# Performance work log

Measured on AMD Instinct MI355X. Metric: run time of the kernel, lower is better.

Reference implementation:

```python
import jax, jax.numpy as jnp
import numpy as np

HEADS = 8
DIM_HEAD = 32
EPS = 1e-5


def setup_inputs() -> dict:
    key = jax.random.key(0)
    ks = jax.random.split(key, 6)
    B, C, N = 2, 256, 2048
    inner = HEADS * DIM_HEAD  # 256
    return {
        "x": jax.random.normal(ks[0], (B, C, N), dtype=jnp.float32),
        "gamma": jnp.ones((C,), dtype=jnp.float32),
        "beta": jnp.zeros((C,), dtype=jnp.float32),
        "wk": jax.random.normal(ks[1], (inner, C // HEADS), dtype=jnp.float32) * 0.05,
        "wq": jax.random.normal(ks[2], (inner, C // HEADS), dtype=jnp.float32) * 0.05,
        "wv": jax.random.normal(ks[3], (inner, C // HEADS), dtype=jnp.float32) * 0.05,
        "wo": jax.random.normal(ks[4], (C, inner), dtype=jnp.float32) * 0.05,
        "bo": jnp.zeros((C,), dtype=jnp.float32),
    }


def reference(x, gamma, beta, wk, wq, wv, wo, bo):
    B, C, N = x.shape
    inner = HEADS * DIM_HEAD
    # BatchNorm1d (training mode: batch stats over B and N per channel)
    mean = jnp.mean(x, axis=(0, 2), keepdims=True)
    var = jnp.mean((x - mean) ** 2, axis=(0, 2), keepdims=True)
    xn = (x - mean) * jax.lax.rsqrt(var + EPS) * gamma[None, :, None] + beta[None, :, None]

    # grouped 1x1 conv1d (groups=HEADS): group g maps C//H input chans -> DIM_HEAD out chans
    xg = xn.reshape(B, HEADS, C // HEADS, N)

    def proj(w):
        w3 = w.reshape(HEADS, DIM_HEAD, C // HEADS)
        return jnp.einsum('hdc,bhcn->bhdn', w3, xg).reshape(B, inner, N)

    k = proj(wk)
    q = proj(wq)
    v = proj(wv)

    # faithful rearrange 'b (d h) n -> b h n d' (d outer, h inner in the channel split)
    def split_heads(t):
        return t.reshape(B, DIM_HEAD, HEADS, N).transpose(0, 2, 3, 1)  # b h n d

    # faithful q/k swap from the original: q<-split(k), k<-split(q), v<-split(v)
    qh, kh, vh = split_heads(k), split_heads(q), split_heads(v)

    scale = DIM_HEAD ** -0.5
    dots = jnp.einsum('bhid,bhjd->bhij', qh, kh) * scale  # [B,H,N,N]
    attn = jax.nn.softmax(dots, axis=-1)
    out = jnp.einsum('bhij,bhjd->bhid', attn, vh)  # [B,H,N,D]

    # rearrange 'b h n d -> b (h d) n'
    out = out.transpose(0, 1, 3, 2).reshape(B, inner, N)
    # output 1x1 conv with bias
    return jnp.einsum('oc,bcn->bon', wo, out) + bo[None, :, None]
```

## Files before the change

### kernel.cpp

```cpp
#include <hip/hip_runtime.h>

#define TID threadIdx.x

constexpr int B = 2, C = 256, N = 2048, H = 8, D = 32, BH = 16;
constexpr float EPS = 1e-5f;
constexpr float SCL2 = 0.25505654344454694f;
constexpr size_t SZ = (size_t)BH * N * D;

typedef _Float16 h8 __attribute__((ext_vector_type(8)));
typedef _Float16 h4 __attribute__((ext_vector_type(4)));
typedef float f32x4 __attribute__((ext_vector_type(4)));

__global__ __launch_bounds__(256) void k_bnstats(const float* __restrict__ x,
                                                 const float* __restrict__ gamma,
                                                 const float* __restrict__ beta,
                                                 float* __restrict__ stats) {
  int c = blockIdx.x;
  float s = 0.f, ss = 0.f;
  const float4* x4 = (const float4*)x;
  for (int k = 0; k < B; ++k) {
    const float4* p = x4 + (size_t)(k * C + c) * (N / 4);
    for (int i = TID; i < N / 4; i += 256) {
      float4 v = p[i];
      s += v.x + v.y + v.z + v.w;
      ss += v.x * v.x + v.y * v.y + v.z * v.z + v.w * v.w;
    }
  }
#pragma unroll
  for (int off = 32; off; off >>= 1) {
    s += __shfl_down(s, off);
    ss += __shfl_down(ss, off);
  }
  __shared__ float red[8];
  int w = TID >> 6;
  if ((TID & 63) == 0) { red[w] = s; red[4 + w] = ss; }
  __syncthreads();
  if (TID == 0) {
    float S = red[0] + red[1] + red[2] + red[3];
    float SS = red[4] + red[5] + red[6] + red[7];
    float mean = S * (1.f / (B * N));
    float var = SS * (1.f / (B * N)) - mean * mean;
    float a = rsqrtf(var + EPS) * gamma[c];
    stats[c] = a;
    stats[C + c] = beta[c] - mean * a;
  }
}

__global__ __launch_bounds__(256) void k_proj(const float* __restrict__ x,
    const float* __restrict__ wk, const float* __restrict__ wq,
    const float* __restrict__ wv, const float* __restrict__ stats,
    _Float16* __restrict__ qa, _Float16* __restrict__ ka, _Float16* __restrict__ va) {
  int proj = blockIdx.x >> 8;
  int rem = blockIdx.x & 255;
  int b = rem >> 7;
  int n0 = (rem & 127) * 16;
  const float* w = proj == 0 ? wk : (proj == 1 ? wq : wv);
  _Float16* out = proj == 0 ? qa : (proj == 1 ? ka : va);

  __shared__ float w_t[32 * 264];
  __shared__ float xs[256 * 18];
  __shared__ float sab[512];

  sab[TID] = stats[TID];
  sab[256 + TID] = stats[256 + TID];
  {
    const float4* wr4 = (const float4*)(w + TID * 32);
#pragma unroll
    for (int p = 0; p < 8; ++p) {
      float4 v = wr4[p];
      w_t[(p * 4 + 0) * 264 + TID] = v.x;
      w_t[(p * 4 + 1) * 264 + TID] = v.y;
      w_t[(p * 4 + 2) * 264 + TID] = v.z;
      w_t[(p * 4 + 3) * 264 + TID] = v.w;
    }
  }
  __syncthreads();
#pragma unroll
  for (int p = 0; p < 4; ++p) {
    int c = p * 64 + (TID >> 2);
    int n4 = (TID & 3) * 4;
    float4 v = *(const float4*)(x + (size_t)(b * C + c) * N + n0 + n4);
    float a = sab[c], bb = sab[256 + c];
    int row = (c >> 5) + ((c & 31) << 3);
    int swz = ((row >> 4) & 3) << 2;
    float2 lo = {v.x * a + bb, v.y * a + bb};
    float2 hi = {v.z * a + bb, v.w * a + bb};
    *(float2*)&xs[row * 18 + (n4 ^ swz)] = lo;
    *(float2*)&xs[row * 18 + ((n4 + 2) ^ swz)] = hi;
  }
  __syncthreads();

  int d = TID & 31, t2 = TID >> 5;
  int g = d >> 2;
  float2 acc[8];
#pragma unroll
  for (int h = 0; h < 8; ++h) acc[h] = (float2){0.f, 0.f};
#pragma unroll
  for (int c = 0; c < 32; ++c) {
    float4 w0 = *(const float4*)&w_t[c * 264 + 8 * d];
    float4 w1 = *(const float4*)&w_t[c * 264 + 8 * d + 4];
    int row = g + 8 * c;
    int swz = ((row >> 4) & 3) << 2;
    float2 xv = *(const float2*)&xs[row * 18 + ((t2 * 2) ^ swz)];
    acc[0].x += w0.x * xv.x; acc[0].y += w0.x * xv.y;
    acc[1].x += w0.y * xv.x; acc[1].y += w0.y * xv.y;
    acc[2].x += w0.z * xv.x; acc[2].y += w0.z * xv.y;
    acc[3].x += w0.w * xv.x; acc[3].y += w0.w * xv.y;
    acc[4].x += w1.x * xv.x; acc[4].y += w1.x * xv.y;
    acc[5].x += w1.y * xv.x; acc[5].y += w1.y * xv.y;
    acc[6].x += w1.z * xv.x; acc[6].y += w1.z * xv.y;
    acc[7].x += w1.w * xv.x; acc[7].y += w1.w * xv.y;
  }
  int n = n0 + t2 * 2;
  if (proj < 2) {
#pragma unroll
    for (int h = 0; h < 8; ++h) {
      size_t o = ((size_t)((b * 8 + h) * N) + n) * D + d;
      out[o] = (_Float16)acc[h].x;
      out[o + D] = (_Float16)acc[h].y;
    }
  } else {
#pragma unroll
    for (int h = 0; h < 8; ++h) {
      size_t o = ((size_t)((b * 8 + h) * D) + d) * N + n;
      out[o] = (_Float16)acc[h].x;
      out[o + 1] = (_Float16)acc[h].y;
    }
  }
}

__global__ __launch_bounds__(256, 4) void k_attn(
    const _Float16* __restrict__ qa, const _Float16* __restrict__ ka,
    const _Float16* __restrict__ va, float* __restrict__ op,
    float* __restrict__ mp, float* __restrict__ lp) {
  int bid = blockIdx.x;
  int r = bid & 7;
  int q = bid >> 3;
  int js = q >> 6;
  int bh = r * 2 + ((q >> 5) & 1);
  int rb = q & 31;
  constexpr int ntiles = 16;

  int w = TID >> 6;
  int lane = TID & 63;
  int il = lane & 15;
  int g = lane >> 4;

  __shared__ char Kc[4096];
  __shared__ char Vc[4096];
  __shared__ char Pc[4 * 2048];
  char* Pw = Pc + w * 2048;

  int n_q = rb * 64 + w * 16 + il;
  h8 qf = *(const h8*)(qa + ((size_t)bh * N + n_q) * D + g * 8);

  f32x4 accO[2];
#pragma unroll
  for (int dh = 0; dh < 2; ++dh) accO[dh] = (f32x4){0.f, 0.f, 0.f, 0.f};
  float m = -3.0e38f, l = 0.f;

  int kj = TID >> 2, kc = TID & 3;
  const _Float16* kbase = ka + ((size_t)bh * N + (size_t)js * 1024 + kj) * D + kc * 8;
  int kdst = (kj * 64 + kc * 16) ^ ((kj & 3) << 4);
  int vd = TID >> 3, vc = TID & 7;
  const _Float16* vbase = va + ((size_t)bh * D + vd) * N + (size_t)js * 1024 + vc * 8;
  int vdst = (vd * 128 + vc * 16) ^ ((vd & 7) << 4) ^ (((vd >> 3) & 3) << 5);

  h8 kreg = *(const h8*)kbase;
  h8 vreg = *(const h8*)vbase;

  for (int t = 0; t < ntiles; ++t) {
    __syncthreads();
    *(h8*)(Kc + kdst) = kreg;
    *(h8*)(Vc + vdst) = vreg;
    if (t + 1 < ntiles) {
      kreg = *(const h8*)(kbase + (size_t)(t + 1) * 64 * D);
      vreg = *(const h8*)(vbase + (t + 1) * 64);
    }
    __syncthreads();

    float pv[4][4];
    float tmax = -3.0e38f;
#pragma unroll
    for (int jt = 0; jt < 4; ++jt) {
      int krow = jt * 16 + il;
      h8 kf = *(const h8*)(Kc + ((krow * 64 + g * 16) ^ ((krow & 3) << 4)));
      f32x4 accS = (f32x4){0.f, 0.f, 0.f, 0.f};
      accS = __builtin_amdgcn_mfma_f32_16x16x32_f16(kf, qf, accS, 0, 0, 0);
#pragma unroll
      for (int e = 0; e < 4; ++e) {
        float xv = accS[e] * SCL2;
        pv[jt][e] = xv;
        tmax = fmaxf(tmax, xv);
      }
    }
    tmax = fmaxf(tmax, __shfl_xor(tmax, 16));
    tmax = fmaxf(tmax, __shfl_xor(tmax, 32));
    float mn = fmaxf(m, tmax);
    float corr = exp2f(m - mn);
    float ls = 0.f;
#pragma unroll
    for (int jt = 0; jt < 4; ++jt)
#pragma unroll
      for (int e = 0; e < 4; ++e) {
        float pe = exp2f(pv[jt][e] - mn);
        pv[jt][e] = pe;
        ls += pe;
      }
    ls += __shfl_xor(ls, 16);
    ls += __shfl_xor(ls, 32);
    l = l * corr + ls;
    m = mn;
#pragma unroll
    for (int dh = 0; dh < 2; ++dh)
#pragma unroll
      for (int e = 0; e < 4; ++e) accO[dh][e] *= corr;

#pragma unroll
    for (int jt = 0; jt < 4; ++jt) {
      h4 ph = {(_Float16)pv[jt][0], (_Float16)pv[jt][1],
               (_Float16)pv[jt][2], (_Float16)pv[jt][3]};
      *(h4*)(Pw + ((il * 128 + jt * 32 + g * 8) ^ ((il & 7) << 4))) = ph;
    }

#pragma unroll
    for (int jb = 0; jb < 2; ++jb) {
      h8 pf = *(const h8*)(Pw + ((il * 128 + jb * 64 + g * 16) ^ ((il & 7) << 4)));
#pragma unroll
      for (int dh = 0; dh < 2; ++dh) {
        int vrow = dh * 16 + il;
        int vaddr = (vrow * 128 + jb * 64 + g * 16) ^ ((vrow & 7) << 4) ^
                    (((vrow >> 3) & 3) << 5);
        h8 vf = *(const h8*)(Vc + vaddr);
        accO[dh] = __builtin_amdgcn_mfma_f32_16x16x32_f16(vf, pf, accO[dh], 0, 0, 0);
      }
    }
  }

  int b = bh >> 3, h = bh & 7;
  size_t obase = ((size_t)((js * 2 + b) * N) + n_q) * C + h * 32;
#pragma unroll
  for (int dh = 0; dh < 2; ++dh) {
    float4 o4 = {accO[dh][0], accO[dh][1], accO[dh][2], accO[dh][3]};
    *(float4*)(op + obase + dh * 16 + g * 4) = o4;
  }
  if (g == 0) {
    size_t idx = (size_t)(js * BH + bh) * N + n_q;
    mp[idx] = m;
    lp[idx] = l;
  }
}

__global__ __launch_bounds__(256) void k_final(const float* __restrict__ op,
    const float* __restrict__ mp, const float* __restrict__ lp,
    const float* __restrict__ wo, const float* __restrict__ bo,
    float* __restrict__ out) {
  __shared__ _Float16 woh[32 * 256];
  __shared__ _Float16 wol[32 * 256];
  __shared__ _Float16 as_[32 * 256];
  __shared__ float cwa[8 * 32], cwb[8 * 32];
  __shared__ float bos[32];
  int nt = blockIdx.x & 63, oq = (blockIdx.x >> 6) & 7, b = blockIdx.x >> 9;
  int n0 = nt * 32, o0 = oq * 32;

  {
    int h = TID >> 5, n_l = TID & 31;
    size_t i0 = (size_t)(b * 8 + h) * N + n0 + n_l;
    size_t i1 = (size_t)(BH + b * 8 + h) * N + n0 + n_l;
    float m0 = mp[i0], m1 = mp[i1];
    float mg = fmaxf(m0, m1);
    float w0 = exp2f(m0 - mg), w1 = exp2f(m1 - mg);
    float inv = 1.f / (w0 * lp[i0] + w1 * lp[i1]);
    cwa[TID] = w0 * inv;
    cwb[TID] = w1 * inv;
  }
  if (TID < 32) bos[TID] = bo[o0 + TID];
  {
    int cc = TID & 63;
    int ob = TID >> 6;
#pragma unroll
    for (int p = 0; p < 8; ++p) {
      int o = ob + p * 4;
      float4 v = ((const float4*)wo)[(o0 + o) * 64 + cc];
      _Float16 h0 = (_Float16)v.x, h1 = (_Float16)v.y,
               h2 = (_Float16)v.z, h3 = (_Float16)v.w;
      h4 hi = {h0, h1, h2, h3};
      h4 lo = {(_Float16)(v.x - (float)h0), (_Float16)(v.y - (float)h1),
               (_Float16)(v.z - (float)h2), (_Float16)(v.w - (float)h3)};
      int byte = (o * 512 + cc * 8) ^ ((o & 7) << 4);
      *(h4*)((char*)woh + byte) = hi;
      *(h4*)((char*)wol + byte) = lo;
    }
  }
  __syncthreads();
  {
    int cc = TID & 63;
    int h = cc >> 3;
    int nb = TID >> 6;
#pragma unroll
    for (int p = 0; p < 8; ++p) {
      int n = nb + p * 4;
      float4 v0 = *(const float4*)(op + ((size_t)(b * N) + n0 + n) * C + cc * 4);
      float4 v1 = *(const float4*)(op + ((size_t)((2 + b) * N) + n0 + n) * C + cc * 4);
      float ca = cwa[h * 32 + n], cb = cwb[h * 32 + n];
      h4 av = {(_Float16)(ca * v0.x + cb * v1.x), (_Float16)(ca * v0.y + cb * v1.y),
               (_Float16)(ca * v0.z + cb * v1.z), (_Float16)(ca * v0.w + cb * v1.w)};
      int byte = (n * 512 + cc * 8) ^ ((n & 7) << 4);
      *(h4*)((char*)as_ + byte) = av;
    }
  }
  __syncthreads();

  int w = TID >> 6, lane = TID & 63, il = lane & 15, g = lane >> 4;
  int ow = (w & 1) * 16, nw = (w >> 1) * 16;
  f32x4 acc = (f32x4){0.f, 0.f, 0.f, 0.f};
#pragma unroll
  for (int ks = 0; ks < 8; ++ks) {
    int abyte = ((nw + il) * 512 + ks * 64 + g * 16) ^ ((il & 7) << 4);
    h8 bf = *(const h8*)((char*)as_ + abyte);
    int wbyte = ((ow + il) * 512 + ks * 64 + g * 16) ^ ((il & 7) << 4);
    h8 ah = *(const h8*)((char*)woh + wbyte);
    h8 al = *(const h8*)((char*)wol + wbyte);
    acc = __builtin_amdgcn_mfma_f32_16x16x32_f16(ah, bf, acc, 0, 0, 0);
    acc = __builtin_amdgcn_mfma_f32_16x16x32_f16(al, bf, acc, 0, 0, 0);
  }
  int n = n0 + nw + il;
#pragma unroll
  for (int r = 0; r < 4; ++r) {
    int o_l = ow + g * 4 + r;
    out[(size_t)(b * C + o0 + o_l) * N + n] = acc[r] + bos[o_l];
  }
}

extern "C" void kernel_launch(void* const* d_in, const int* in_sizes, int n_in,
                              void* d_out, int out_size, void* d_ws, size_t ws_size,
                              hipStream_t stream) {
  const float* x = (const float*)d_in[0];
  const float* gamma = (const float*)d_in[1];
  const float* beta = (const float*)d_in[2];
  const float* wk = (const float*)d_in[3];
  const float* wq = (const float*)d_in[4];
  const float* wv = (const float*)d_in[5];
  const float* wo = (const float*)d_in[6];
  const float* bo = (const float*)d_in[7];
  float* out = (float*)d_out;
  float* ws = (float*)d_ws;

  float* stats = ws;
  _Float16* qa = (_Float16*)(ws + 1024);
  _Float16* ka = qa + SZ;
  _Float16* va = ka + SZ;
  float* op = (float*)(va + SZ);
  float* mp = op + 2 * SZ;
  float* lp = mp + 2 * (size_t)BH * N;

  k_bnstats<<<256, 256, 0, stream>>>(x, gamma, beta, stats);
  k_proj<<<768, 256, 0, stream>>>(x, wk, wq, wv, stats, qa, ka, va);
  k_attn<<<1024, 256, 0, stream>>>(qa, ka, va, op, mp, lp);
  k_final<<<1024, 256, 0, stream>>>(op, mp, lp, wo, bo, out);
}
```

Measured before the change: 61.85 us.

## Double-buffer K/V tiles and feed P to MFMA from registers via permuted K layout

K and V tiles in shared memory become double-buffered, so each iteration needs one barrier instead of two, and the next tile is stored after compute. The P staging buffer in LDS is removed. K rows are stored in a permuted order so each lane's softmax probabilities already match the B-operand layout of the PV MFMA, which lets the probabilities be packed directly from registers. This removes LDS writes and reads for P and one sync per tile, at the cost of more shared memory for K/V and dependence on the permutation being exactly right.

```diff
diff --git a/kernel.cpp b/kernel.cpp
--- a/kernel.cpp
+++ b/kernel.cpp
@@ -146,10 +146,8 @@
   int il = lane & 15;
   int g = lane >> 4;
 
-  __shared__ char Kc[4096];
-  __shared__ char Vc[4096];
-  __shared__ char Pc[4 * 2048];
-  char* Pw = Pc + w * 2048;
+  __shared__ char Kc[2][4096];
+  __shared__ char Vc[2][4096];
 
   int n_q = rb * 64 + w * 16 + il;
   h8 qf = *(const h8*)(qa + ((size_t)bh * N + n_q) * D + g * 8);
@@ -160,31 +158,33 @@
   float m = -3.0e38f, l = 0.f;
 
   int kj = TID >> 2, kc = TID & 3;
+  int pk = ((kj >> 5) * 2 + ((kj >> 2) & 1)) * 16 + ((kj >> 3) & 3) * 4 + (kj & 3);
   const _Float16* kbase = ka + ((size_t)bh * N + (size_t)js * 1024 + kj) * D + kc * 8;
-  int kdst = (kj * 64 + kc * 16) ^ ((kj & 3) << 4);
+  int kdst = (pk * 64 + kc * 16) ^ ((pk & 3) << 4);
   int vd = TID >> 3, vc = TID & 7;
   const _Float16* vbase = va + ((size_t)bh * D + vd) * N + (size_t)js * 1024 + vc * 8;
   int vdst = (vd * 128 + vc * 16) ^ ((vd & 7) << 4) ^ (((vd >> 3) & 3) << 5);
 
   h8 kreg = *(const h8*)kbase;
   h8 vreg = *(const h8*)vbase;
+  *(h8*)(Kc[0] + kdst) = kreg;
+  *(h8*)(Vc[0] + vdst) = vreg;
+  __syncthreads();
 
   for (int t = 0; t < ntiles; ++t) {
-    __syncthreads();
-    *(h8*)(Kc + kdst) = kreg;
-    *(h8*)(Vc + vdst) = vreg;
-    if (t + 1 < ntiles) {
+    int cur = t & 1;
+    bool more = (t + 1 < ntiles);
+    if (more) {
       kreg = *(const h8*)(kbase + (size_t)(t + 1) * 64 * D);
       vreg = *(const h8*)(vbase + (t + 1) * 64);
     }
-    __syncthreads();
 
     float pv[4][4];
     float tmax = -3.0e38f;
 #pragma unroll
     for (int jt = 0; jt < 4; ++jt) {
       int krow = jt * 16 + il;
-      h8 kf = *(const h8*)(Kc + ((krow * 64 + g * 16) ^ ((krow & 3) << 4)));
+      h8 kf = *(const h8*)(Kc[cur] + ((krow * 64 + g * 16) ^ ((krow & 3) << 4)));
       f32x4 accS = (f32x4){0.f, 0.f, 0.f, 0.f};
       accS = __builtin_amdgcn_mfma_f32_16x16x32_f16(kf, qf, accS, 0, 0, 0);
 #pragma unroll
@@ -217,23 +217,25 @@
       for (int e = 0; e < 4; ++e) accO[dh][e] *= corr;
 
 #pragma unroll
-    for (int jt = 0; jt < 4; ++jt) {
-      h4 ph = {(_Float16)pv[jt][0], (_Float16)pv[jt][1],
-               (_Float16)pv[jt][2], (_Float16)pv[jt][3]};
-      *(h4*)(Pw + ((il * 128 + jt * 32 + g * 8) ^ ((il & 7) << 4))) = ph;
-    }
-
-#pragma unroll
     for (int jb = 0; jb < 2; ++jb) {
-      h8 pf = *(const h8*)(Pw + ((il * 128 + jb * 64 + g * 16) ^ ((il & 7) << 4)));
+      h8 pf = {(_Float16)pv[2 * jb][0],     (_Float16)pv[2 * jb][1],
+               (_Float16)pv[2 * jb][2],     (_Float16)pv[2 * jb][3],
+               (_Float16)pv[2 * jb + 1][0], (_Float16)pv[2 * jb + 1][1],
+               (_Float16)pv[2 * jb + 1][2], (_Float16)pv[2 * jb + 1][3]};
 #pragma unroll
       for (int dh = 0; dh < 2; ++dh) {
         int vrow = dh * 16 + il;
         int vaddr = (vrow * 128 + jb * 64 + g * 16) ^ ((vrow & 7) << 4) ^
                     (((vrow >> 3) & 3) << 5);
-        h8 vf = *(const h8*)(Vc + vaddr);
+        h8 vf = *(const h8*)(Vc[cur] + vaddr);
         accO[dh] = __builtin_amdgcn_mfma_f32_16x16x32_f16(vf, pf, accO[dh], 0, 0, 0);
       }
+    }
+
+    if (more) {
+      *(h8*)(Kc[cur ^ 1] + kdst) = kreg;
+      *(h8*)(Vc[cur ^ 1] + vdst) = vreg;
+      __syncthreads();
     }
   }
 
```

After: 60.68 us. Within noise of the previous version (-1.9%).
